# Performance work log

Hardware: AMD Instinct MI355X
Metric: run time of the kernel (lower is better)

## Reference

```python
import jax, jax.numpy as jnp
import numpy as np

NEG_BIG = -9e15
ALPHA = 0.2  # leaky relu slope


def setup_inputs() -> dict:
    key = jax.random.key(0)
    k1, k2, k3, k4 = jax.random.split(key, 4)
    B, N, Fin, Fout = 8, 2048, 128, 64
    h = jax.random.normal(k1, (B, N, Fin), dtype=jnp.float32)
    adj = jax.random.randint(k2, (B, N, N), 0, 2, dtype=jnp.int32)
    # xavier_uniform-like init scale
    W = jax.random.uniform(k3, (Fin, Fout), dtype=jnp.float32, minval=-1.0, maxval=1.0) * (1.414 * np.sqrt(6.0 / (Fin + Fout)))
    a = jax.random.uniform(k4, (2 * Fout, 1), dtype=jnp.float32, minval=-1.0, maxval=1.0) * (1.414 * np.sqrt(6.0 / (2 * Fout + 1)))
    return {"h": h, "adj": adj, "W": W, "a": a}


def reference(h, adj, W, a):
    # h: [B,N,Fin], adj: [B,N,N], W: [Fin,Fout], a: [2*Fout,1]
    Fout = W.shape[1]
    Wh = jnp.einsum('bni,io->bno', h, W)            # [B,N,Fout]
    # e_ij = leakyrelu(a[:Fout] . Wh_i + a[Fout:] . Wh_j)  (decomposed, same math
    # as the original concat + matmul with a)
    f_src = Wh @ a[:Fout, 0]                        # [B,N]
    f_dst = Wh @ a[Fout:, 0]                        # [B,N]
    e = f_src[:, :, None] + f_dst[:, None, :]       # [B,N,N]
    e = jnp.where(e > 0, e, ALPHA * e)              # leaky relu
    e = jnp.where(adj > 0, e, NEG_BIG)              # mask
    attention = jax.nn.softmax(e, axis=2)           # [B,N,N]
    h_prime = jnp.einsum('bnm,bmo->bno', attention, Wh)
    return jax.nn.elu(h_prime)
```

## Files before the change

### kernel.cpp

```cpp
#include <hip/hip_runtime.h>
#include <hip/hip_bf16.h>

constexpr int Bb  = 8;
constexpr int Nn  = 2048;
constexpr int FIN = 128;
constexpr int FOUT = 64;
constexpr float LOG2E = 1.4426950408889634f;

typedef __bf16 bf16x8 __attribute__((ext_vector_type(8)));
typedef __bf16 bf16x2 __attribute__((ext_vector_type(2)));
typedef float  f32x4  __attribute__((ext_vector_type(4)));
typedef unsigned int u32;
typedef unsigned long long u64;

__device__ __forceinline__ u32 f2bf_bits(float f) {
    u32 u = __builtin_bit_cast(u32, f);
    return (u + 0x7FFFu + ((u >> 16) & 1u)) >> 16;
}

__global__ __launch_bounds__(256) void gat_k01(
        const float* __restrict__ h, const int* __restrict__ adj,
        const float* __restrict__ W, const float* __restrict__ a,
        __bf16* __restrict__ whfrag, float* __restrict__ fs,
        float* __restrict__ fd, u64* __restrict__ mask) {
    __shared__ __align__(16) float hT[32][FIN];

    const int l = threadIdx.x & 63;
    const int w = __builtin_amdgcn_readfirstlane((int)(threadIdx.x >> 6));

    if (blockIdx.x >= 512) {
        const size_t gw = (size_t)(blockIdx.x - 512) * 4 + w;
        const int* p   = adj + gw * 4096 + l;
        u64* mout      = mask + gw * 64;
#pragma unroll 1
        for (int i = 0; i < 64; i += 8) {
            int v[8];
#pragma unroll
            for (int k = 0; k < 8; ++k) v[k] = p[(i + k) * 64];
            u64 m[8];
#pragma unroll
            for (int k = 0; k < 8; ++k) m[k] = __ballot(v[k] > 0);
            if (l == 0) {
#pragma unroll
                for (int k = 0; k < 8; ++k) mout[i + k] = m[k];
            }
        }
        return;
    }

    const int blk = blockIdx.x;
    const int b   = blk >> 6;
    const int t32 = blk & 63;
    const int n0  = t32 * 32;

    {
        const float4* hb = reinterpret_cast<const float4*>(h + (size_t)(b * Nn + n0) * FIN);
        float4* dst = reinterpret_cast<float4*>(&hT[0][0]);
#pragma unroll
        for (int k = 0; k < 4; ++k) {
            const int flat = threadIdx.x + k * 256;
            dst[flat] = hb[flat];
        }
    }
    __syncthreads();

    const float a0 = a[l];
    const float a1 = a[FOUT + l];

    float acc[8];
#pragma unroll
    for (int r = 0; r < 8; ++r) acc[r] = 0.f;

#pragma unroll 1
    for (int c0 = 0; c0 < FIN; c0 += 32) {
        float wreg[32];
#pragma unroll
        for (int cc = 0; cc < 32; ++cc) wreg[cc] = W[(c0 + cc) * FOUT + l];
#pragma unroll
        for (int r = 0; r < 8; ++r) {
            const int row = w * 8 + r;
#pragma unroll
            for (int cc = 0; cc < 32; ++cc)
                acc[r] = fmaf(hT[row][c0 + cc], wreg[cc], acc[r]);
        }
    }

#pragma unroll
    for (int r = 0; r < 8; ++r) {
        float s0 = acc[r] * a0;
        float s1 = acc[r] * a1;
#pragma unroll
        for (int off = 32; off >= 1; off >>= 1) {
            s0 += __shfl_xor(s0, off, 64);
            s1 += __shfl_xor(s1, off, 64);
        }
        if (l == 0) {
            fs[b * Nn + n0 + w * 8 + r] = s0 * LOG2E;
            fd[b * Nn + n0 + w * 8 + r] = s1 * LOG2E;
        }
    }

    u32 pk[4];
#pragma unroll
    for (int i = 0; i < 4; ++i)
        pk[i] = f2bf_bits(acc[2 * i]) | (f2bf_bits(acc[2 * i + 1]) << 16);
    const int slotg = ((b * 64 + t32) * 4 + (l >> 4)) * 64 + ((w << 4) | (l & 15));
    reinterpret_cast<uint4*>(whfrag)[slotg] = make_uint4(pk[0], pk[1], pk[2], pk[3]);
}

__global__ __launch_bounds__(256, 4) void gat_k2(
        const u64* __restrict__ mask, const __bf16* __restrict__ whfrag,
        const float* __restrict__ fs, const float* __restrict__ fd,
        float* __restrict__ out) {
    const int blk = blockIdx.x;
    const int b   = blk >> 7;
    const int i0  = (blk & 127) * 16;
    const int l   = threadIdx.x & 63;
    const int w   = __builtin_amdgcn_readfirstlane((int)(threadIdx.x >> 6));

    __shared__ __align__(16) char  aLDS[4 * 4096];
    __shared__ f32x4 comb[4][4][64];
    __shared__ float zpart[4][16];

    const int g  = l >> 4;
    const int jc = l & 15;
    const int shl = jc * 4;

    char* myA = aLDS + w * 4096;

    float fs_loc[4];
#pragma unroll
    for (int rr = 0; rr < 4; ++rr) fs_loc[rr] = fs[b * Nn + i0 + g * 4 + rr];

    const int    jq0  = w * 512;
    const float* fdp  = fd + b * Nn + jq0 + jc * 4;
    const u64*   mkp  = mask + (size_t)(b * Nn + i0 + g * 4) * 32 + w * 8;

    const bf16x8* bfr = reinterpret_cast<const bf16x8*>(whfrag)
                        + (size_t)((b * 64 + w * 16) * 4) * 64 + l;

    f32x4 acc[4] = {{0,0,0,0},{0,0,0,0},{0,0,0,0},{0,0,0,0}};
    f32x4 accz   = {0.f, 0.f, 0.f, 0.f};

    bf16x8 onesv;
#pragma unroll
    for (int i = 0; i < 8; ++i) onesv[i] = (__bf16)1.0f;

    u64   maskR[3][4];
    f32x4 fdR[3];

#pragma unroll
    for (int rr = 0; rr < 4; ++rr) {
        maskR[0][rr] = mkp[rr * 32 + 0];
        maskR[1][rr] = mkp[rr * 32 + 1];
    }
    fdR[0] = *reinterpret_cast<const f32x4*>(fdp);
    fdR[1] = *reinterpret_cast<const f32x4*>(fdp + 64);

#define GAT_STEP(IT, CUR, PRE)                                                 \
  {                                                                            \
    if ((IT) + 2 < 8) {                \
      _Pragma("unroll")                                                        \
      for (int rr = 0; rr < 4; ++rr)                                           \
        maskR[PRE][rr] = mkp[rr * 32 + (IT) + 2];                              \
      fdR[PRE] = *reinterpret_cast<const f32x4*>(fdp + ((IT) + 2) * 64);       \
    }                                                                          \
    char* buf = myA + ((IT) & 1) * 2048;                                       \
    _Pragma("unroll")                                                          \
    for (int rr = 0; rr < 4; ++rr) {                                           \
      const int row = g * 4 + rr;                                              \
      const u32 mm = (u32)(maskR[CUR][rr] >> shl);  \
      u32 wds[2];                                                              \
      _Pragma("unroll")                                                        \
      for (int hp = 0; hp < 2; ++hp) {                                         \
        float pv[2];                                                           \
        _Pragma("unroll")                                                      \
        for (int q = 0; q < 2; ++q) {                                          \
          const int jj = hp * 2 + q;                                           \
          float e  = fs_loc[rr] + fdR[CUR][jj];                                \
          float lr = fmaxf(e, 0.2f * e);          \
          float p  = exp2f(lr);                 \
          pv[q] = ((mm >> jj) & 1u) ? p : 0.f;                                 \
        }                                                                      \
        wds[hp] = __builtin_bit_cast(u32,                                      \
                      (bf16x2){(__bf16)pv[0], (__bf16)pv[1]});                 \
      }                                                                        \
      const int boff = (row * 128 + jc * 8) ^ ((row & 7) << 4);                \
      *reinterpret_cast<uint2*>(buf + boff) = make_uint2(wds[0], wds[1]);      \
    }                                                                          \
    asm volatile("s_waitcnt lgkmcnt(0)" ::: "memory");                         \
    __builtin_amdgcn_sched_barrier(0x20);            \
    {                                                                          \
      const int rb0 = (((l & 15) * 128 + g * 16) ^ ((l & 7) << 4));            \
      bf16x8 av = *reinterpret_cast<const bf16x8*>(buf + rb0);                 \
      _Pragma("unroll")                                                        \
      for (int o16 = 0; o16 < 4; ++o16)                                        \
        acc[o16] = __builtin_amdgcn_mfma_f32_16x16x32_bf16(                    \
            av, bfr[(((IT) * 2 + 0) * 4 + o16) * 64], acc[o16], 0, 0, 0);      \
      accz = __builtin_amdgcn_mfma_f32_16x16x32_bf16(av, onesv, accz, 0, 0, 0);\
    }                                                                          \
    {                                                                          \
      const int rb1 = (((l & 15) * 128 + 64 + g * 16) ^ ((l & 7) << 4));       \
      bf16x8 av = *reinterpret_cast<const bf16x8*>(buf + rb1);                 \
      _Pragma("unroll")                                                        \
      for (int o16 = 0; o16 < 4; ++o16)                                        \
        acc[o16] = __builtin_amdgcn_mfma_f32_16x16x32_bf16(                    \
            av, bfr[(((IT) * 2 + 1) * 4 + o16) * 64], acc[o16], 0, 0, 0);      \
      accz = __builtin_amdgcn_mfma_f32_16x16x32_bf16(av, onesv, accz, 0, 0, 0);\
    }                                                                          \
  }

    GAT_STEP(0, 0, 2)
    GAT_STEP(1, 1, 0)
    GAT_STEP(2, 2, 1)
    GAT_STEP(3, 0, 2)
    GAT_STEP(4, 1, 0)
    GAT_STEP(5, 2, 1)
    GAT_STEP(6, 0, 2)
    GAT_STEP(7, 1, 0)
#undef GAT_STEP

    if ((l & 15) == 0) {
#pragma unroll
        for (int r = 0; r < 4; ++r) zpart[w][(l >> 4) * 4 + r] = accz[r];
    }
#pragma unroll
    for (int o16 = 0; o16 < 4; ++o16) comb[w][o16][l] = acc[o16];
    __syncthreads();

    f32x4 res = comb[0][w][l];
#pragma unroll
    for (int wp = 1; wp < 4; ++wp) res += comb[wp][w][l];

#pragma unroll
    for (int r = 0; r < 4; ++r) {
        const int row = g * 4 + r;
        float z = zpart[0][row] + zpart[1][row] + zpart[2][row] + zpart[3][row];
        float v = res[r] / z;
        v = v > 0.f ? v : expm1f(v);
        out[(size_t)(b * Nn + i0 + row) * FOUT + w * 16 + jc] = v;
    }
}

extern "C" void kernel_launch(void* const* d_in, const int* in_sizes, int n_in,
                              void* d_out, int out_size, void* d_ws, size_t ws_size,
                              hipStream_t stream) {
    const float* h   = (const float*)d_in[0];
    const int*   adj = (const int*)d_in[1];
    const float* W   = (const float*)d_in[2];
    const float* a   = (const float*)d_in[3];
    float* out = (float*)d_out;

    __bf16* whfrag = (__bf16*)d_ws;
    float*  fs     = (float*)((char*)d_ws + (size_t)Bb * Nn * FOUT * 2);
    float*  fd     = fs + Bb * Nn;
    u64*    mask   = (u64*)((char*)d_ws + (4u << 20));

    gat_k01<<<dim3(512 + 2048), dim3(256), 0, stream>>>(h, adj, W, a, whfrag, fs, fd, mask);
    gat_k2 <<<dim3(Bb * 128),   dim3(256), 0, stream>>>(mask, whfrag, fs, fd, out);
}
```

Baseline: 52.08 us.

## Widen adjacency-mask loads and retile attention kernel to 32 rows over 8 waves

The mask-building path now reads adjacency with 16-byte vector loads and assembles the 64-bit masks through lane shuffles, replacing per-element loads and ballots. The attention kernel moves from 16-row blocks of 4 waves to 32-row blocks of 8 waves. Each wave covers 256 columns and feeds two 16-row MFMA tiles, so every Wh fragment it loads is reused twice. The trade-offs are higher LDS use (64KB per block), fewer blocks in total, and an 8-way cross-wave reduction at the end.

```diff
diff --git a/kernel.cpp b/kernel.cpp
--- a/kernel.cpp
+++ b/kernel.cpp
@@ -10,6 +10,7 @@
 typedef __bf16 bf16x8 __attribute__((ext_vector_type(8)));
 typedef __bf16 bf16x2 __attribute__((ext_vector_type(2)));
 typedef float  f32x4  __attribute__((ext_vector_type(4)));
+typedef int    i32x4  __attribute__((ext_vector_type(4)));
 typedef unsigned int u32;
 typedef unsigned long long u64;
 
@@ -30,20 +31,24 @@
 
     if (blockIdx.x >= 512) {
         const size_t gw = (size_t)(blockIdx.x - 512) * 4 + w;
-        const int* p   = adj + gw * 4096 + l;
-        u64* mout      = mask + gw * 64;
-#pragma unroll 1
-        for (int i = 0; i < 64; i += 8) {
-            int v[8];
-#pragma unroll
-            for (int k = 0; k < 8; ++k) v[k] = p[(i + k) * 64];
-            u64 m[8];
-#pragma unroll
-            for (int k = 0; k < 8; ++k) m[k] = __ballot(v[k] > 0);
-            if (l == 0) {
-#pragma unroll
-                for (int k = 0; k < 8; ++k) mout[i + k] = m[k];
-            }
+        const int* p  = adj + gw * 4096 + 4 * l;
+        u64* mout     = mask + gw * 64;
+        i32x4 vv[2];
+        vv[0] = *reinterpret_cast<const i32x4*>(p);
+#pragma unroll
+        for (int i = 0; i < 16; ++i) {
+            const int cur = i & 1;
+            if (i < 15)
+                vv[cur ^ 1] = *reinterpret_cast<const i32x4*>(p + (i + 1) * 256);
+            const i32x4 v = vv[cur];
+            u32 nib = (v[0] > 0 ? 1u : 0u) | (v[1] > 0 ? 2u : 0u) |
+                      (v[2] > 0 ? 4u : 0u) | (v[3] > 0 ? 8u : 0u);
+            u32 x = nib | (((u32)__shfl_xor((int)nib, 1)) << 4);
+            x |= ((u32)__shfl_xor((int)x, 2)) << 8;
+            x |= ((u32)__shfl_xor((int)x, 4)) << 16;
+            u32 hi = (u32)__shfl_xor((int)x, 8);
+            if ((l & 15) == 0)
+                mout[i * 4 + (l >> 4)] = (u64)x | ((u64)hi << 32);
         }
         return;
     }
@@ -108,137 +113,146 @@
     reinterpret_cast<uint4*>(whfrag)[slotg] = make_uint4(pk[0], pk[1], pk[2], pk[3]);
 }
 
-__global__ __launch_bounds__(256, 4) void gat_k2(
+__global__ __launch_bounds__(512, 4) void gat_k2(
         const u64* __restrict__ mask, const __bf16* __restrict__ whfrag,
         const float* __restrict__ fs, const float* __restrict__ fd,
         float* __restrict__ out) {
     const int blk = blockIdx.x;
-    const int b   = blk >> 7;
-    const int i0  = (blk & 127) * 16;
+    const int b   = blk >> 6;
+    const int i0  = (blk & 63) * 32;
     const int l   = threadIdx.x & 63;
     const int w   = __builtin_amdgcn_readfirstlane((int)(threadIdx.x >> 6));
 
-    __shared__ __align__(16) char  aLDS[4 * 4096];
-    __shared__ f32x4 comb[4][4][64];
-    __shared__ float zpart[4][16];
-
-    const int g  = l >> 4;
-    const int jc = l & 15;
+    __shared__ __align__(16) char smem[64 * 1024];
+    __shared__ float zpart[8][32];
+
+    const int g   = l >> 4;
+    const int jc  = l & 15;
     const int shl = jc * 4;
 
-    char* myA = aLDS + w * 4096;
-
-    float fs_loc[4];
-#pragma unroll
-    for (int rr = 0; rr < 4; ++rr) fs_loc[rr] = fs[b * Nn + i0 + g * 4 + rr];
-
-    const int    jq0  = w * 512;
-    const float* fdp  = fd + b * Nn + jq0 + jc * 4;
-    const u64*   mkp  = mask + (size_t)(b * Nn + i0 + g * 4) * 32 + w * 8;
+    char* myA = smem + w * 8192;
+
+    float fs_loc[2][4];
+#pragma unroll
+    for (int hh = 0; hh < 2; ++hh)
+#pragma unroll
+        for (int rr = 0; rr < 4; ++rr)
+            fs_loc[hh][rr] = fs[b * Nn + i0 + hh * 16 + g * 4 + rr];
+
+    const float* fdp = fd + b * Nn + w * 256 + jc * 4;
+    const u64*   mkp = mask + (size_t)(b * Nn + i0 + g * 4) * 32 + w * 4;
 
     const bf16x8* bfr = reinterpret_cast<const bf16x8*>(whfrag)
-                        + (size_t)((b * 64 + w * 16) * 4) * 64 + l;
-
-    f32x4 acc[4] = {{0,0,0,0},{0,0,0,0},{0,0,0,0},{0,0,0,0}};
-    f32x4 accz   = {0.f, 0.f, 0.f, 0.f};
+                        + (size_t)((b * 64 + w * 8) * 4) * 64 + l;
+
+    f32x4 acc[2][4] = {{{0,0,0,0},{0,0,0,0},{0,0,0,0},{0,0,0,0}},
+                       {{0,0,0,0},{0,0,0,0},{0,0,0,0},{0,0,0,0}}};
+    f32x4 accz[2]   = {{0,0,0,0},{0,0,0,0}};
 
     bf16x8 onesv;
 #pragma unroll
     for (int i = 0; i < 8; ++i) onesv[i] = (__bf16)1.0f;
 
-    u64   maskR[3][4];
-    f32x4 fdR[3];
-
-#pragma unroll
-    for (int rr = 0; rr < 4; ++rr) {
-        maskR[0][rr] = mkp[rr * 32 + 0];
-        maskR[1][rr] = mkp[rr * 32 + 1];
-    }
+    u64   maskR[2][2][4];
+    f32x4 fdR[2];
+
+#pragma unroll
+    for (int hh = 0; hh < 2; ++hh)
+#pragma unroll
+        for (int rr = 0; rr < 4; ++rr)
+            maskR[0][hh][rr] = mkp[hh * 512 + rr * 32];
     fdR[0] = *reinterpret_cast<const f32x4*>(fdp);
-    fdR[1] = *reinterpret_cast<const f32x4*>(fdp + 64);
-
-#define GAT_STEP(IT, CUR, PRE)                                                 \
+
+#define GAT_STEP(IT, CUR, NXT)                                                 \
   {                                                                            \
-    if ((IT) + 2 < 8) {                \
+    if ((IT) + 1 < 4) {                                                        \
       _Pragma("unroll")                                                        \
-      for (int rr = 0; rr < 4; ++rr)                                           \
-        maskR[PRE][rr] = mkp[rr * 32 + (IT) + 2];                              \
-      fdR[PRE] = *reinterpret_cast<const f32x4*>(fdp + ((IT) + 2) * 64);       \
+      for (int hh = 0; hh < 2; ++hh)                                           \
+        _Pragma("unroll")                                                      \
+        for (int rr = 0; rr < 4; ++rr)                                         \
+          maskR[NXT][hh][rr] = mkp[hh * 512 + rr * 32 + (IT) + 1];             \
+      fdR[NXT] = *reinterpret_cast<const f32x4*>(fdp + ((IT) + 1) * 64);       \
     }                                                                          \
-    char* buf = myA + ((IT) & 1) * 2048;                                       \
+    char* buf = myA + ((IT) & 1) * 4096;                                       \
     _Pragma("unroll")                                                          \
-    for (int rr = 0; rr < 4; ++rr) {                                           \
-      const int row = g * 4 + rr;                                              \
-      const u32 mm = (u32)(maskR[CUR][rr] >> shl);  \
-      u32 wds[2];                                                              \
+    for (int hh = 0; hh < 2; ++hh) {                                           \
       _Pragma("unroll")                                                        \
-      for (int hp = 0; hp < 2; ++hp) {                                         \
-        float pv[2];                                                           \
+      for (int rr = 0; rr < 4; ++rr) {                                         \
+        const int row = hh * 16 + g * 4 + rr;                                  \
+        const u32 mm = (u32)(maskR[CUR][hh][rr] >> shl);                       \
+        u32 wds[2];                                                            \
         _Pragma("unroll")                                                      \
-        for (int q = 0; q < 2; ++q) {                                          \
-          const int jj = hp * 2 + q;                                           \
-          float e  = fs_loc[rr] + fdR[CUR][jj];                                \
-          float lr = fmaxf(e, 0.2f * e);          \
-          float p  = exp2f(lr);                 \
-          pv[q] = ((mm >> jj) & 1u) ? p : 0.f;                                 \
+        for (int hp = 0; hp < 2; ++hp) {                                       \
+          float pv[2];                                                         \
+          _Pragma("unroll")                                                    \
+          for (int q = 0; q < 2; ++q) {                                        \
+            const int jj = hp * 2 + q;                                         \
+            float e  = fs_loc[hh][rr] + fdR[CUR][jj];                          \
+            float lr = fmaxf(e, 0.2f * e);        \
+            float p  = exp2f(lr);                  \
+            pv[q] = ((mm >> jj) & 1u) ? p : 0.f;                               \
+          }                                                                    \
+          wds[hp] = __builtin_bit_cast(u32,                                    \
+                        (bf16x2){(__bf16)pv[0], (__bf16)pv[1]});               \
         }                                                                      \
-        wds[hp] = __builtin_bit_cast(u32,                                      \
-                      (bf16x2){(__bf16)pv[0], (__bf16)pv[1]});                 \
+        const int boff = (row * 128 + jc * 8) ^ ((row & 7) << 4);              \
+        *reinterpret_cast<uint2*>(buf + boff) = make_uint2(wds[0], wds[1]);    \
       }                                                                        \
-      const int boff = (row * 128 + jc * 8) ^ ((row & 7) << 4);                \
-      *reinterpret_cast<uint2*>(buf + boff) = make_uint2(wds[0], wds[1]);      \
     }                                                                          \
     asm volatile("s_waitcnt lgkmcnt(0)" ::: "memory");                         \
     __builtin_amdgcn_sched_barrier(0x20);            \
-    {                                                                          \
-      const int rb0 = (((l & 15) * 128 + g * 16) ^ ((l & 7) << 4));            \
-      bf16x8 av = *reinterpret_cast<const bf16x8*>(buf + rb0);                 \
+    _Pragma("unroll")                                                          \
+    for (int kb = 0; kb < 2; ++kb) {                                           \
       _Pragma("unroll")                                                        \
-      for (int o16 = 0; o16 < 4; ++o16)                                        \
-        acc[o16] = __builtin_amdgcn_mfma_f32_16x16x32_bf16(                    \
-            av, bfr[(((IT) * 2 + 0) * 4 + o16) * 64], acc[o16], 0, 0, 0);      \
-      accz = __builtin_amdgcn_mfma_f32_16x16x32_bf16(av, onesv, accz, 0, 0, 0);\
-    }                                                                          \
-    {                                                                          \
-      const int rb1 = (((l & 15) * 128 + 64 + g * 16) ^ ((l & 7) << 4));       \
-      bf16x8 av = *reinterpret_cast<const bf16x8*>(buf + rb1);                 \
-      _Pragma("unroll")                                                        \
-      for (int o16 = 0; o16 < 4; ++o16)                                        \
-        acc[o16] = __builtin_amdgcn_mfma_f32_16x16x32_bf16(                    \
-            av, bfr[(((IT) * 2 + 1) * 4 + o16) * 64], acc[o16], 0, 0, 0);      \
-      accz = __builtin_amdgcn_mfma_f32_16x16x32_bf16(av, onesv, accz, 0, 0, 0);\
+      for (int hh = 0; hh < 2; ++hh) {                                         \
+        const int rb = (((hh * 16 + (l & 15)) * 128 + kb * 64 + (l >> 4) * 16) \
+                        ^ ((l & 7) << 4));                                     \
+        bf16x8 av = *reinterpret_cast<const bf16x8*>(buf + rb);                \
+        _Pragma("unroll")                                                      \
+        for (int o16 = 0; o16 < 4; ++o16)                                      \
+          acc[hh][o16] = __builtin_amdgcn_mfma_f32_16x16x32_bf16(              \
+              av, bfr[(((IT) * 2 + kb) * 4 + o16) * 64], acc[hh][o16], 0,0,0); \
+        accz[hh] = __builtin_amdgcn_mfma_f32_16x16x32_bf16(                    \
+              av, onesv, accz[hh], 0, 0, 0);                                   \
+      }                                                                        \
     }                                                                          \
   }
 
-    GAT_STEP(0, 0, 2)
+    GAT_STEP(0, 0, 1)
     GAT_STEP(1, 1, 0)
-    GAT_STEP(2, 2, 1)
-    GAT_STEP(3, 0, 2)
-    GAT_STEP(4, 1, 0)
-    GAT_STEP(5, 2, 1)
-    GAT_STEP(6, 0, 2)
-    GAT_STEP(7, 1, 0)
+    GAT_STEP(2, 0, 1)
+    GAT_STEP(3, 1, 0)
 #undef GAT_STEP
 
     if ((l & 15) == 0) {
 #pragma unroll
-        for (int r = 0; r < 4; ++r) zpart[w][(l >> 4) * 4 + r] = accz[r];
-    }
-#pragma unroll
-    for (int o16 = 0; o16 < 4; ++o16) comb[w][o16][l] = acc[o16];
+        for (int hh = 0; hh < 2; ++hh)
+#pragma unroll
+            for (int r = 0; r < 4; ++r)
+                zpart[w][hh * 16 + (l >> 4) * 4 + r] = accz[hh][r];
+    }
+    f32x4* comb = reinterpret_cast<f32x4*>(smem);
+#pragma unroll
+    for (int hh = 0; hh < 2; ++hh)
+#pragma unroll
+        for (int o16 = 0; o16 < 4; ++o16)
+            comb[w * 512 + (o16 * 2 + hh) * 64 + l] = acc[hh][o16];
     __syncthreads();
 
-    f32x4 res = comb[0][w][l];
-#pragma unroll
-    for (int wp = 1; wp < 4; ++wp) res += comb[wp][w][l];
+    const int ow = w & 3, eh = w >> 2;
+    f32x4 res = comb[(ow * 2 + eh) * 64 + l];
+#pragma unroll
+    for (int wp = 1; wp < 8; ++wp) res += comb[wp * 512 + (ow * 2 + eh) * 64 + l];
 
 #pragma unroll
     for (int r = 0; r < 4; ++r) {
-        const int row = g * 4 + r;
-        float z = zpart[0][row] + zpart[1][row] + zpart[2][row] + zpart[3][row];
+        const int row = eh * 16 + (l >> 4) * 4 + r;
+        float z = 0.f;
+#pragma unroll
+        for (int wp = 0; wp < 8; ++wp) z += zpart[wp][row];
         float v = res[r] / z;
         v = v > 0.f ? v : expm1f(v);
-        out[(size_t)(b * Nn + i0 + row) * FOUT + w * 16 + jc] = v;
+        out[(size_t)(b * Nn + i0 + row) * FOUT + ow * 16 + (l & 15)] = v;
     }
 }
 
@@ -257,5 +271,5 @@
     u64*    mask   = (u64*)((char*)d_ws + (4u << 20));
 
     gat_k01<<<dim3(512 + 2048), dim3(256), 0, stream>>>(h, adj, W, a, whfrag, fs, fd, mask);
-    gat_k2 <<<dim3(Bb * 128),   dim3(256), 0, stream>>>(mask, whfrag, fs, fd, out);
-}
+    gat_k2 <<<dim3(512),        dim3(512), 0, stream>>>(mask, whfrag, fs, fd, out);
+}
```

Measured after the change: 56.89 us. 1.09x slower.
